# Performance work log

Hardware: AMD Instinct MI355X
Metric: run time of the kernel (lower is better)

The kernel has to match this reference:

```python
import jax, jax.numpy as jnp
import numpy as np

N = 50000      # nodes
E = 800000     # edges (before self-loops)
G = 128        # graphs in batch
IN = 128       # input_dim
H = 4          # heads
D = 32         # hidden_dim per head (H*D = 128)
L = 3          # n_layers
COND = 7       # data.stats features
LAT = 32       # latent_dim
NEG_SLOPE = 0.2


def setup_inputs() -> dict:
    key = jax.random.key(0)
    ks = jax.random.split(key, 10)
    s = 0.1
    return {
        "x": jax.random.normal(ks[0], (N, IN), jnp.float32),
        "cond": jax.random.normal(ks[1], (G, COND), jnp.float32),
        "W": jax.random.normal(ks[2], (L, IN, H * D), jnp.float32) * s,
        "a_src": jax.random.normal(ks[3], (L, H, D), jnp.float32) * s,
        "a_dst": jax.random.normal(ks[4], (L, H, D), jnp.float32) * s,
        "conv_bias": jnp.zeros((L, H * D), jnp.float32),
        "bn_gamma": jnp.ones((H * D + COND,), jnp.float32),
        "bn_beta": jnp.zeros((H * D + COND,), jnp.float32),
        "fc_w": jax.random.normal(ks[5], (H * D + COND, LAT), jnp.float32) * s,
        "fc_b": jnp.zeros((LAT,), jnp.float32),
        "edge_index": jax.random.randint(ks[6], (2, E), 0, N, jnp.int32),
        "batch": jnp.sort(jax.random.randint(ks[7], (N,), 0, G, jnp.int32)),
    }


def _leaky(x, slope):
    return jnp.where(x > 0, x, slope * x)


def _gat_layer(x, W, a_s, a_d, b, src, dst):
    # x: [N, F_in] -> h: [N, H, D]
    h = (x @ W).reshape(N, H, D)
    al_s = jnp.einsum("nhd,hd->nh", h, a_s)   # [N, H]
    al_d = jnp.einsum("nhd,hd->nh", h, a_d)   # [N, H]
    e = _leaky(al_s[src] + al_d[dst], NEG_SLOPE)          # [Etot, H]
    m = jax.ops.segment_max(e, dst, num_segments=N)       # per-dst max
    ex = jnp.exp(e - m[dst])
    denom = jax.ops.segment_sum(ex, dst, num_segments=N)  # [N, H]
    alpha = ex / (denom[dst] + 1e-16)                     # softmax over in-edges
    out = jax.ops.segment_sum(alpha[:, :, None] * h[src], dst, num_segments=N)
    return out.reshape(N, H * D) + b


def reference(x, cond, W, a_src, a_dst, conv_bias, bn_gamma, bn_beta, fc_w, fc_b,
              edge_index, batch):
    loops = jnp.arange(N, dtype=edge_index.dtype)  # PyG GATConv adds self-loops
    src = jnp.concatenate([edge_index[0], loops])
    dst = jnp.concatenate([edge_index[1], loops])
    for i in range(L):
        x = _gat_layer(x, W[i], a_src[i], a_dst[i], conv_bias[i], src, dst)
        x = _leaky(x, 0.2)  # encoder's LeakyReLU(0.2); dropout skipped (eval)
    pooled = jax.ops.segment_sum(x, batch, num_segments=G)  # global_add_pool
    out = jnp.concatenate([pooled, cond], axis=1)           # [G, H*D+7]
    mu = out.mean(axis=0)
    var = out.var(axis=0)                                   # biased, as torch BN
    out = (out - mu) / jnp.sqrt(var + 1e-5) * bn_gamma + bn_beta
    return out @ fc_w + fc_b                                # [G, LAT]
```

## Files before the change

### kernel.cpp

```cpp
#include <hip/hip_runtime.h>
#include <math.h>

#define N_NODES 50000
#define N_EDGES 800000
#define ETOT (N_EDGES + N_NODES)
#define G_GRAPHS 128
#define HD 128
#define COND_F 7
#define NFEAT 135
#define LAT 32
#define L_LAYERS 3
#define SLOPE 0.2f
#define MAXDEG 96
#define N_TEAMS 8
#define TEAM_RANGE ((N_NODES + N_TEAMS - 1) / N_TEAMS)
#define SC_BLOCKS (N_TEAMS * 416)

typedef __attribute__((ext_vector_type(8))) short bf16x8;
typedef __attribute__((ext_vector_type(4))) float f32x4;

__device__ __forceinline__ float leaky_(float x) { return x > 0.f ? x : SLOPE * x; }

__device__ __forceinline__ unsigned short f2bf_(float f) {
    unsigned int u = __float_as_uint(f);
    u += 0x7FFF + ((u >> 16) & 1);
    return (unsigned short)(u >> 16);
}
__device__ __forceinline__ float bf2f_(unsigned short b) {
    return __uint_as_float((unsigned int)b << 16);
}
__device__ __forceinline__ unsigned int pack_bf2_(float lo, float hi) {
    unsigned int ulo = __float_as_uint(lo); ulo += 0x7FFF + ((ulo >> 16) & 1);
    unsigned int uhi = __float_as_uint(hi); uhi += 0x7FFF + ((uhi >> 16) & 1);
    return (ulo >> 16) | (uhi & 0xFFFF0000u);
}

__global__ __launch_bounds__(256) void scatter_kernel(const int* __restrict__ ei,
                                                      int* __restrict__ fill,
                                                      int* __restrict__ csr) {
    int team = blockIdx.x & (N_TEAMS - 1);
    int bt = blockIdx.x >> 3;
    int nbt = gridDim.x >> 3;
    int tid = bt * blockDim.x + threadIdx.x;
    int stride = nbt * blockDim.x;
    int lo = team * TEAM_RANGE;
    int hi = min(lo + TEAM_RANGE, N_NODES);
    for (int i = tid; i < ETOT; i += stride) {
        int dstv = (i < N_EDGES) ? ei[N_EDGES + i] : (i - N_EDGES);
        if (dstv >= lo && dstv < hi) {
            int srcv = (i < N_EDGES) ? ei[i] : dstv;
            int slot = atomicAdd(&fill[dstv], 1);
            if (slot < MAXDEG) csr[slot * N_NODES + dstv] = srcv;
        }
    }
}

__global__ void prep_kernel(const float* __restrict__ W, const float* __restrict__ a_s,
                            const float* __restrict__ a_d, unsigned short* __restrict__ Wt,
                            unsigned short* __restrict__ Wa) {
    int i = blockIdx.x * blockDim.x + threadIdx.x;
    const int NW = L_LAYERS * 128 * 128;
    if (i < NW) {
        int l = i >> 14, rem = i & 16383, k = rem >> 7, n = rem & 127;
        unsigned int u = __float_as_uint(W[i]);
        u += 0x7FFF + ((u >> 16) & 1);
        Wt[(l << 14) + n * 128 + k] = (unsigned short)(u >> 16);
        return;
    }
    int j = i - NW;
    if (j >= L_LAYERS * 16 * 128) return;
    int l = j >> 11, rem = j & 2047, c = rem >> 7, k = rem & 127;
    float v = 0.f;
    if (c < 8) {
        int h = c >> 1;
        const float* av = (c & 1) ? &a_d[l * 128 + h * 32] : &a_s[l * 128 + h * 32];
        const float* wrow = &W[(l << 14) + k * 128 + h * 32];
#pragma unroll
        for (int d = 0; d < 32; ++d) v = fmaf(wrow[d], av[d], v);
    }
    Wa[j] = f2bf_(v);
}

__global__ __launch_bounds__(256) void gemm_mfma_kernel(
    const float* __restrict__ x, const unsigned short* __restrict__ Wt,
    const unsigned short* __restrict__ Wa,
    unsigned short* __restrict__ h_bf, float* __restrict__ al_s,
    float* __restrict__ al_d) {
    __shared__ __align__(16) unsigned short xs[64 * 128];
    int t = threadIdx.x;
    int lane = t & 63;
    int w = t >> 6;
    int row0 = blockIdx.x * 64;

    {
        int r = t >> 2, c0 = (t & 3) * 32;
        int gr = row0 + r;
        unsigned int upk[16];
        if (gr < N_NODES) {
            const float* src = &x[(size_t)gr * 128 + c0];
#pragma unroll
            for (int i = 0; i < 8; ++i) {
                float4 v = *(const float4*)&src[i * 4];
                upk[i * 2 + 0] = pack_bf2_(v.x, v.y);
                upk[i * 2 + 1] = pack_bf2_(v.z, v.w);
            }
        } else {
#pragma unroll
            for (int i = 0; i < 16; ++i) upk[i] = 0;
        }
        char* base = (char*)xs + r * 256;
#pragma unroll
        for (int i = 0; i < 4; ++i) {
            int cb = c0 * 2 + i * 16;
            int sw = cb ^ ((r & 7) << 4);
            *(uint4*)(base + sw) = make_uint4(upk[i * 4 + 0], upk[i * 4 + 1],
                                              upk[i * 4 + 2], upk[i * 4 + 3]);
        }
    }
    int l15 = lane & 15, g16 = lane >> 4;
    int cn = w * 32;
    bf16x8 bfr[2][4];
#pragma unroll
    for (int ct = 0; ct < 2; ++ct)
#pragma unroll
        for (int ks = 0; ks < 4; ++ks)
            bfr[ct][ks] = *(const bf16x8*)&Wt[(size_t)(cn + ct * 16 + l15) * 128 + ks * 32 + g16 * 8];
    bf16x8 bfrL[4];
    if (w == 0) {
#pragma unroll
        for (int ks = 0; ks < 4; ++ks)
            bfrL[ks] = *(const bf16x8*)&Wa[l15 * 128 + ks * 32 + g16 * 8];
    }
    __syncthreads();

    f32x4 acc[4][2];
    f32x4 accL[4];
#pragma unroll
    for (int rt = 0; rt < 4; ++rt) {
#pragma unroll
        for (int ct = 0; ct < 2; ++ct) acc[rt][ct] = (f32x4){0.f, 0.f, 0.f, 0.f};
        accL[rt] = (f32x4){0.f, 0.f, 0.f, 0.f};
    }

#pragma unroll
    for (int ks = 0; ks < 4; ++ks) {
        bf16x8 af[4];
#pragma unroll
        for (int rt = 0; rt < 4; ++rt) {
            int r = rt * 16 + l15;
            int cb = ks * 64 + g16 * 16;
            af[rt] = *(const bf16x8*)((const char*)xs + r * 256 + (cb ^ ((r & 7) << 4)));
        }
#pragma unroll
        for (int rt = 0; rt < 4; ++rt)
#pragma unroll
            for (int ct = 0; ct < 2; ++ct)
                acc[rt][ct] = __builtin_amdgcn_mfma_f32_16x16x32_bf16(
                    af[rt], bfr[ct][ks], acc[rt][ct], 0, 0, 0);
        if (w == 0) {
#pragma unroll
            for (int rt = 0; rt < 4; ++rt)
                accL[rt] = __builtin_amdgcn_mfma_f32_16x16x32_bf16(
                    af[rt], bfrL[ks], accL[rt], 0, 0, 0);
        }
    }

    __syncthreads();

#pragma unroll
    for (int rt = 0; rt < 4; ++rt) {
#pragma unroll
        for (int j = 0; j < 4; ++j) {
            int r = rt * 16 + g16 * 4 + j;
            int sw = (r & 7) << 4;
            char* rowb = (char*)xs + r * 256;
            *(unsigned short*)(rowb + (((cn + l15) * 2) ^ sw)) = f2bf_(acc[rt][0][j]);
            *(unsigned short*)(rowb + (((cn + 16 + l15) * 2) ^ sw)) = f2bf_(acc[rt][1][j]);
        }
    }
    if (w == 0) {
#pragma unroll
        for (int rt = 0; rt < 4; ++rt) {
#pragma unroll
            for (int j = 0; j < 4; ++j) {
                int grow = row0 + rt * 16 + g16 * 4 + j;
                if (l15 < 8 && grow < N_NODES) {
                    float v = accL[rt][j];
                    if (l15 & 1) al_d[grow * 4 + (l15 >> 1)] = v;
                    else al_s[grow * 4 + (l15 >> 1)] = v;
                }
            }
        }
    }
    __syncthreads();
#pragma unroll
    for (int i = 0; i < 4; ++i) {
        int flat = i * 4096 + t * 16;
        int r = flat >> 8;
        int cb = flat & 255;
        uint4 v = *(const uint4*)((const char*)xs + r * 256 + (cb ^ ((r & 7) << 4)));
        int gr = row0 + r;
        if (gr < N_NODES)
            *(uint4*)((char*)&h_bf[(size_t)gr * 128] + cb) = v;
    }
}

__global__ __launch_bounds__(256) void agg_kernel(
    const unsigned short* __restrict__ h_bf, const float* __restrict__ al_s,
    const float* __restrict__ al_d, const int* __restrict__ deg_arr,
    const int* __restrict__ csr, const float* __restrict__ bias,
    float* __restrict__ xout) {
    __shared__ float alph[4][64][4];
    __shared__ int srcs[4][64];
    __shared__ float bounce[4][160];
    int wslot = threadIdx.x >> 6;
    int wv = (blockIdx.x * blockDim.x + threadIdx.x) >> 6;
    int lane = threadIdx.x & 63;
    if (wv >= N_NODES) return;
    int node = wv;
    int deg = min(deg_arr[node], MAXDEG);
    float4 ad = *(const float4*)&al_d[node * 4];

    if (deg <= 64) {
        float e0 = -1e30f, e1 = -1e30f, e2 = -1e30f, e3 = -1e30f;
        int s_l = 0;
        if (lane < deg) {
            s_l = csr[lane * N_NODES + node];
            float4 as = *(const float4*)&al_s[s_l * 4];
            e0 = leaky_(as.x + ad.x);
            e1 = leaky_(as.y + ad.y);
            e2 = leaky_(as.z + ad.z);
            e3 = leaky_(as.w + ad.w);
        }
        float m0 = e0, m1 = e1, m2 = e2, m3 = e3;
#pragma unroll
        for (int off = 1; off < 64; off <<= 1) {
            m0 = fmaxf(m0, __shfl_xor(m0, off));
            m1 = fmaxf(m1, __shfl_xor(m1, off));
            m2 = fmaxf(m2, __shfl_xor(m2, off));
            m3 = fmaxf(m3, __shfl_xor(m3, off));
        }
        float x0 = 0.f, x1 = 0.f, x2 = 0.f, x3 = 0.f;
        if (lane < deg) {
            x0 = __expf(e0 - m0);
            x1 = __expf(e1 - m1);
            x2 = __expf(e2 - m2);
            x3 = __expf(e3 - m3);
        }
        float d0 = x0, d1 = x1, d2 = x2, d3 = x3;
#pragma unroll
        for (int off = 1; off < 64; off <<= 1) {
            d0 += __shfl_xor(d0, off);
            d1 += __shfl_xor(d1, off);
            d2 += __shfl_xor(d2, off);
            d3 += __shfl_xor(d3, off);
        }
        float i0 = 1.f / (d0 + 1e-16f), i1 = 1.f / (d1 + 1e-16f);
        float i2 = 1.f / (d2 + 1e-16f), i3 = 1.f / (d3 + 1e-16f);

        *(float4*)&alph[wslot][lane][0] =
            make_float4(x0 * i0, x1 * i1, x2 * i2, x3 * i3);
        srcs[wslot][lane] = s_l;

        int grp = lane >> 4, li = lane & 15;
        int hq = li >> 2;
        float facc[8];
#pragma unroll
        for (int k = 0; k < 8; ++k) facc[k] = 0.f;
        int degr = (deg + 3) & ~3;
        int j0 = 0;
        for (; j0 + 8 <= degr; j0 += 8) {
            int eA = j0 + grp, eB = j0 + 4 + grp;
            int sA = srcs[wslot][eA];
            int sB = srcs[wslot][eB];
            float aA = alph[wslot][eA][hq];
            float aB = alph[wslot][eB][hq];
            uint4 vA = *(const uint4*)&h_bf[(size_t)sA * 128 + li * 8];
            uint4 vB = *(const uint4*)&h_bf[(size_t)sB * 128 + li * 8];
            facc[0] = fmaf(aA, __uint_as_float(vA.x << 16), facc[0]);
            facc[1] = fmaf(aA, __uint_as_float(vA.x & 0xFFFF0000u), facc[1]);
            facc[2] = fmaf(aA, __uint_as_float(vA.y << 16), facc[2]);
            facc[3] = fmaf(aA, __uint_as_float(vA.y & 0xFFFF0000u), facc[3]);
            facc[4] = fmaf(aA, __uint_as_float(vA.z << 16), facc[4]);
            facc[5] = fmaf(aA, __uint_as_float(vA.z & 0xFFFF0000u), facc[5]);
            facc[6] = fmaf(aA, __uint_as_float(vA.w << 16), facc[6]);
            facc[7] = fmaf(aA, __uint_as_float(vA.w & 0xFFFF0000u), facc[7]);
            facc[0] = fmaf(aB, __uint_as_float(vB.x << 16), facc[0]);
            facc[1] = fmaf(aB, __uint_as_float(vB.x & 0xFFFF0000u), facc[1]);
            facc[2] = fmaf(aB, __uint_as_float(vB.y << 16), facc[2]);
            facc[3] = fmaf(aB, __uint_as_float(vB.y & 0xFFFF0000u), facc[3]);
            facc[4] = fmaf(aB, __uint_as_float(vB.z << 16), facc[4]);
            facc[5] = fmaf(aB, __uint_as_float(vB.z & 0xFFFF0000u), facc[5]);
            facc[6] = fmaf(aB, __uint_as_float(vB.w << 16), facc[6]);
            facc[7] = fmaf(aB, __uint_as_float(vB.w & 0xFFFF0000u), facc[7]);
        }
        if (j0 < degr) {
            int e = j0 + grp;
            int s = srcs[wslot][e];
            float a = alph[wslot][e][hq];
            uint4 v = *(const uint4*)&h_bf[(size_t)s * 128 + li * 8];
            facc[0] = fmaf(a, __uint_as_float(v.x << 16), facc[0]);
            facc[1] = fmaf(a, __uint_as_float(v.x & 0xFFFF0000u), facc[1]);
            facc[2] = fmaf(a, __uint_as_float(v.y << 16), facc[2]);
            facc[3] = fmaf(a, __uint_as_float(v.y & 0xFFFF0000u), facc[3]);
            facc[4] = fmaf(a, __uint_as_float(v.z << 16), facc[4]);
            facc[5] = fmaf(a, __uint_as_float(v.z & 0xFFFF0000u), facc[5]);
            facc[6] = fmaf(a, __uint_as_float(v.w << 16), facc[6]);
            facc[7] = fmaf(a, __uint_as_float(v.w & 0xFFFF0000u), facc[7]);
        }
#pragma unroll
        for (int k = 0; k < 8; ++k) {
            facc[k] += __shfl_xor(facc[k], 16);
            facc[k] += __shfl_xor(facc[k], 32);
        }
        if (grp == 0) {
#pragma unroll
            for (int k = 0; k < 8; ++k) bounce[wslot][k * 17 + li] = facc[k];
        }
        int fA = lane, fB = lane + 64;
        float o0 = bounce[wslot][(fA & 7) * 17 + (fA >> 3)];
        float o1 = bounce[wslot][(fB & 7) * 17 + (fB >> 3)];
        xout[node * 128 + fA] = leaky_(o0 + bias[fA]);
        xout[node * 128 + fB] = leaky_(o1 + bias[fB]);
    } else {
        int f0 = lane, f1 = lane + 64;
        int hA = lane >> 5;
        float acc0 = 0.f, acc1 = 0.f;
        float m0 = -1e30f, m1 = -1e30f, m2 = -1e30f, m3 = -1e30f;
        for (int e = lane; e < deg; e += 64) {
            int s = csr[e * N_NODES + node];
            float4 as = *(const float4*)&al_s[s * 4];
            m0 = fmaxf(m0, leaky_(as.x + ad.x));
            m1 = fmaxf(m1, leaky_(as.y + ad.y));
            m2 = fmaxf(m2, leaky_(as.z + ad.z));
            m3 = fmaxf(m3, leaky_(as.w + ad.w));
        }
#pragma unroll
        for (int off = 1; off < 64; off <<= 1) {
            m0 = fmaxf(m0, __shfl_xor(m0, off));
            m1 = fmaxf(m1, __shfl_xor(m1, off));
            m2 = fmaxf(m2, __shfl_xor(m2, off));
            m3 = fmaxf(m3, __shfl_xor(m3, off));
        }
        float d0 = 0.f, d1 = 0.f, d2 = 0.f, d3 = 0.f;
        for (int e = lane; e < deg; e += 64) {
            int s = csr[e * N_NODES + node];
            float4 as = *(const float4*)&al_s[s * 4];
            d0 += __expf(leaky_(as.x + ad.x) - m0);
            d1 += __expf(leaky_(as.y + ad.y) - m1);
            d2 += __expf(leaky_(as.z + ad.z) - m2);
            d3 += __expf(leaky_(as.w + ad.w) - m3);
        }
#pragma unroll
        for (int off = 1; off < 64; off <<= 1) {
            d0 += __shfl_xor(d0, off);
            d1 += __shfl_xor(d1, off);
            d2 += __shfl_xor(d2, off);
            d3 += __shfl_xor(d3, off);
        }
        float i0 = 1.f / (d0 + 1e-16f), i1 = 1.f / (d1 + 1e-16f);
        float i2 = 1.f / (d2 + 1e-16f), i3 = 1.f / (d3 + 1e-16f);
        float adA = hA ? ad.y : ad.x, adB = hA ? ad.w : ad.z;
        float mA = hA ? m1 : m0, mB = hA ? m3 : m2;
        float iA = hA ? i1 : i0, iB = hA ? i3 : i2;
        for (int e = 0; e < deg; ++e) {
            int s = csr[e * N_NODES + node];
            float asA = al_s[s * 4 + hA];
            float asB = al_s[s * 4 + 2 + hA];
            float aA = __expf(leaky_(asA + adA) - mA) * iA;
            float aB = __expf(leaky_(asB + adB) - mB) * iB;
            acc0 = fmaf(aA, bf2f_(h_bf[s * 128 + f0]), acc0);
            acc1 = fmaf(aB, bf2f_(h_bf[s * 128 + f1]), acc1);
        }
        xout[node * 128 + f0] = leaky_(acc0 + bias[f0]);
        xout[node * 128 + f1] = leaky_(acc1 + bias[f1]);
    }
}

#define POOL_CHUNK 128
__global__ __launch_bounds__(256) void pool_kernel(const float* __restrict__ x,
                                                   const int* __restrict__ batch,
                                                   float* __restrict__ pooled) {
    int wv = (blockIdx.x * blockDim.x + threadIdx.x) >> 6;
    int lane = threadIdx.x & 63;
    int n0 = wv * POOL_CHUNK;
    if (n0 >= N_NODES) return;
    int n1 = min(n0 + POOL_CHUNK, N_NODES);
    float a0 = 0.f, a1 = 0.f;
    int gcur = batch[n0];
    for (int n = n0; n < n1; ++n) {
        int g = batch[n];
        if (g != gcur) {
            atomicAdd(&pooled[gcur * 128 + lane], a0);
            atomicAdd(&pooled[gcur * 128 + 64 + lane], a1);
            a0 = a1 = 0.f;
            gcur = g;
        }
        a0 += x[n * 128 + lane];
        a1 += x[n * 128 + 64 + lane];
    }
    atomicAdd(&pooled[gcur * 128 + lane], a0);
    atomicAdd(&pooled[gcur * 128 + 64 + lane], a1);
}

__global__ __launch_bounds__(256) void bnfc_kernel(
    const float* __restrict__ pooled, const float* __restrict__ cond,
    const float* __restrict__ gamma, const float* __restrict__ beta,
    const float* __restrict__ fcw, const float* __restrict__ fcb,
    float* __restrict__ out) {
    __shared__ float Y[G_GRAPHS * NFEAT];
    __shared__ float scale[NFEAT], shift[NFEAT];
    int t = threadIdx.x;
    for (int idx = t; idx < G_GRAPHS * NFEAT; idx += 256) {
        int g = idx / NFEAT, f = idx % NFEAT;
        Y[idx] = (f < HD) ? pooled[g * HD + f] : cond[g * COND_F + (f - HD)];
    }
    __syncthreads();
    if (t < NFEAT) {
        float s = 0.f;
        for (int g = 0; g < G_GRAPHS; ++g) s += Y[g * NFEAT + t];
        float mean = s * (1.f / G_GRAPHS);
        float v = 0.f;
        for (int g = 0; g < G_GRAPHS; ++g) {
            float dd = Y[g * NFEAT + t] - mean;
            v += dd * dd;
        }
        v *= (1.f / G_GRAPHS);
        float inv = rsqrtf(v + 1e-5f);
        float sc = gamma[t] * inv;
        scale[t] = sc;
        shift[t] = beta[t] - mean * sc;
    }
    __syncthreads();
    for (int idx = t; idx < G_GRAPHS * NFEAT; idx += 256) {
        int f = idx % NFEAT;
        Y[idx] = Y[idx] * scale[f] + shift[f];
    }
    __syncthreads();
    for (int idx = t; idx < G_GRAPHS * LAT; idx += 256) {
        int g = idx >> 5, j = idx & 31;
        float acc = fcb[j];
        for (int f = 0; f < NFEAT; ++f) acc = fmaf(Y[g * NFEAT + f], fcw[f * LAT + j], acc);
        out[idx] = acc;
    }
}

extern "C" void kernel_launch(void* const* d_in, const int* in_sizes, int n_in,
                              void* d_out, int out_size, void* d_ws, size_t ws_size,
                              hipStream_t stream) {
    const float* x_in = (const float*)d_in[0];
    const float* cond = (const float*)d_in[1];
    const float* W = (const float*)d_in[2];
    const float* a_src = (const float*)d_in[3];
    const float* a_dst = (const float*)d_in[4];
    const float* conv_bias = (const float*)d_in[5];
    const float* bn_gamma = (const float*)d_in[6];
    const float* bn_beta = (const float*)d_in[7];
    const float* fc_w = (const float*)d_in[8];
    const float* fc_b = (const float*)d_in[9];
    const int* edge_index = (const int*)d_in[10];
    const int* batch = (const int*)d_in[11];
    float* out = (float*)d_out;

    char* ws = (char*)d_ws;
    size_t off = 0;
    auto alloc = [&](size_t bytes) {
        void* p = ws + off;
        off += (bytes + 255) & ~(size_t)255;
        return p;
    };
    float* bufP = (float*)alloc((size_t)N_NODES * 128 * 4);
    unsigned short* h_bf = (unsigned short*)alloc((size_t)N_NODES * 128 * 2);
    unsigned short* Wt = (unsigned short*)alloc((size_t)L_LAYERS * 128 * 128 * 2);
    unsigned short* Wa = (unsigned short*)alloc((size_t)L_LAYERS * 16 * 128 * 2);
    float* als = (float*)alloc((size_t)N_NODES * 4 * 4);
    float* ald = (float*)alloc((size_t)N_NODES * 4 * 4);
    float* pooled = (float*)alloc((size_t)G_GRAPHS * HD * 4);
    int* fill = (int*)alloc((size_t)N_NODES * 4);
    int* csr = (int*)alloc((size_t)N_NODES * MAXDEG * 4);

    hipMemsetAsync(fill, 0, N_NODES * 4, stream);
    hipMemsetAsync(pooled, 0, G_GRAPHS * HD * 4, stream);
    const int NPREP = L_LAYERS * 128 * 128 + L_LAYERS * 16 * 128;
    prep_kernel<<<(NPREP + 255) / 256, 256, 0, stream>>>(W, a_src, a_dst, Wt, Wa);
    scatter_kernel<<<SC_BLOCKS, 256, 0, stream>>>(edge_index, fill, csr);

    const float* xcur = x_in;
    for (int l = 0; l < L_LAYERS; ++l) {
        gemm_mfma_kernel<<<(N_NODES + 63) / 64, 256, 0, stream>>>(
            xcur, Wt + (size_t)l * 128 * 128, Wa + (size_t)l * 16 * 128,
            h_bf, als, ald);
        agg_kernel<<<N_NODES / 4, 256, 0, stream>>>(
            h_bf, als, ald, fill, csr, conv_bias + l * 128, bufP);
        xcur = bufP;
    }

    int pool_waves = (N_NODES + POOL_CHUNK - 1) / POOL_CHUNK;
    pool_kernel<<<(pool_waves + 3) / 4, 256, 0, stream>>>(xcur, batch, pooled);
    bnfc_kernel<<<1, 256, 0, stream>>>(pooled, cond, bn_gamma, bn_beta, fc_w, fc_b, out);
}
```

Measured before the change: 305.8 us.

## Switch CSR to node-major layout and vectorize edge index reads in scatter

The padded CSR is changed from slot-major (slot*N+node) to node-major (node*MAXDEG+slot), so each aggregation wavefront reads its neighbour list as one contiguous span instead of scattered strided words. The scatter kernel now loads destination indices four at a time as int4 and handles self-loops in a separate loop over each team's node range. The store pattern in scatter becomes more scattered per edge, and the int4 path assumes the edge count is a multiple of four.

```diff
diff --git a/kernel.cpp b/kernel.cpp
--- a/kernel.cpp
+++ b/kernel.cpp
@@ -45,13 +45,31 @@
     int stride = nbt * blockDim.x;
     int lo = team * TEAM_RANGE;
     int hi = min(lo + TEAM_RANGE, N_NODES);
-    for (int i = tid; i < ETOT; i += stride) {
-        int dstv = (i < N_EDGES) ? ei[N_EDGES + i] : (i - N_EDGES);
-        if (dstv >= lo && dstv < hi) {
-            int srcv = (i < N_EDGES) ? ei[i] : dstv;
-            int slot = atomicAdd(&fill[dstv], 1);
-            if (slot < MAXDEG) csr[slot * N_NODES + dstv] = srcv;
-        }
+    const int4* d4 = (const int4*)(ei + N_EDGES);
+    const int nv = N_EDGES / 4;
+    for (int i = tid; i < nv; i += stride) {
+        int4 d = d4[i];
+        int idx = i * 4;
+        if (d.x >= lo && d.x < hi) {
+            int s = atomicAdd(&fill[d.x], 1);
+            if (s < MAXDEG) csr[d.x * MAXDEG + s] = ei[idx + 0];
+        }
+        if (d.y >= lo && d.y < hi) {
+            int s = atomicAdd(&fill[d.y], 1);
+            if (s < MAXDEG) csr[d.y * MAXDEG + s] = ei[idx + 1];
+        }
+        if (d.z >= lo && d.z < hi) {
+            int s = atomicAdd(&fill[d.z], 1);
+            if (s < MAXDEG) csr[d.z * MAXDEG + s] = ei[idx + 2];
+        }
+        if (d.w >= lo && d.w < hi) {
+            int s = atomicAdd(&fill[d.w], 1);
+            if (s < MAXDEG) csr[d.w * MAXDEG + s] = ei[idx + 3];
+        }
+    }
+    for (int d = lo + tid; d < hi; d += stride) {
+        int s = atomicAdd(&fill[d], 1);
+        if (s < MAXDEG) csr[d * MAXDEG + s] = d;
     }
 }
 
@@ -219,13 +237,14 @@
     if (wv >= N_NODES) return;
     int node = wv;
     int deg = min(deg_arr[node], MAXDEG);
+    int beg = node * MAXDEG;
     float4 ad = *(const float4*)&al_d[node * 4];
 
     if (deg <= 64) {
         float e0 = -1e30f, e1 = -1e30f, e2 = -1e30f, e3 = -1e30f;
         int s_l = 0;
         if (lane < deg) {
-            s_l = csr[lane * N_NODES + node];
+            s_l = csr[beg + lane];
             float4 as = *(const float4*)&al_s[s_l * 4];
             e0 = leaky_(as.x + ad.x);
             e1 = leaky_(as.y + ad.y);
@@ -326,9 +345,10 @@
         int f0 = lane, f1 = lane + 64;
         int hA = lane >> 5;
         float acc0 = 0.f, acc1 = 0.f;
+        int end = beg + deg;
         float m0 = -1e30f, m1 = -1e30f, m2 = -1e30f, m3 = -1e30f;
-        for (int e = lane; e < deg; e += 64) {
-            int s = csr[e * N_NODES + node];
+        for (int e = beg + lane; e < end; e += 64) {
+            int s = csr[e];
             float4 as = *(const float4*)&al_s[s * 4];
             m0 = fmaxf(m0, leaky_(as.x + ad.x));
             m1 = fmaxf(m1, leaky_(as.y + ad.y));
@@ -343,8 +363,8 @@
             m3 = fmaxf(m3, __shfl_xor(m3, off));
         }
         float d0 = 0.f, d1 = 0.f, d2 = 0.f, d3 = 0.f;
-        for (int e = lane; e < deg; e += 64) {
-            int s = csr[e * N_NODES + node];
+        for (int e = beg + lane; e < end; e += 64) {
+            int s = csr[e];
             float4 as = *(const float4*)&al_s[s * 4];
             d0 += __expf(leaky_(as.x + ad.x) - m0);
             d1 += __expf(leaky_(as.y + ad.y) - m1);
@@ -363,8 +383,8 @@
         float adA = hA ? ad.y : ad.x, adB = hA ? ad.w : ad.z;
         float mA = hA ? m1 : m0, mB = hA ? m3 : m2;
         float iA = hA ? i1 : i0, iB = hA ? i3 : i2;
-        for (int e = 0; e < deg; ++e) {
-            int s = csr[e * N_NODES + node];
+        for (int e = beg; e < end; ++e) {
+            int s = csr[e];
             float asA = al_s[s * 4 + hA];
             float asB = al_s[s * 4 + 2 + hA];
             float aA = __expf(leaky_(asA + adA) - mA) * iA;
```

Measured after the change: 305.2 us. Within noise of the previous version (-0.2%).
